# Kernel optimization log

Measured on AMD Instinct MI355X. Metric: run time of the kernel, lower is better.

## Reference

```python
import jax, jax.numpy as jnp
import numpy as np

N = 262144   # total nodes
E = 1048576  # total edges
B = 512      # graphs per batch
IN, H, EDIM, AH, CH, NB = 8, 128, 4, 128, 128, 4

def _lin(key, fi, fo):
    # kaiming_normal fan_out/relu approximated with fan_in scaling (only affects init stats)
    return jax.random.normal(key, (fi, fo), jnp.float32) * np.sqrt(2.0 / fi)

def setup_inputs() -> dict:
    key = jax.random.key(0)
    ks = jax.random.split(key, 24)
    inp = {}
    inp['x'] = jax.random.normal(ks[0], (N, IN), jnp.float32)
    inp['edge_index'] = jax.random.randint(ks[1], (2, E), 0, N)
    inp['edge_attr'] = jax.random.normal(ks[2], (E, EDIM), jnp.float32)
    seg = N // B
    inp['batch'] = (jnp.arange(N) // seg).astype(jnp.int32)
    inp['ptr'] = (jnp.arange(B + 1) * seg).astype(jnp.int32)
    dims = [(IN, H), (H, H), (H, H)]  # final layer outputs embed_dim == H
    for l, (di, do) in enumerate(dims):
        inp[f'We{l}'] = _lin(ks[3 + 2 * l], EDIM, di)
        inp[f'be{l}'] = jnp.zeros((di,), jnp.float32)
        inp[f'W{l}'] = _lin(ks[4 + 2 * l], di, do)
        inp[f'b{l}'] = jnp.zeros((do,), jnp.float32)
    inp['laW1'] = _lin(ks[10], H, AH); inp['lab1'] = jnp.zeros((AH,), jnp.float32)
    inp['laW2'] = _lin(ks[11], AH, 1); inp['lab2'] = jnp.zeros((1,), jnp.float32)
    inp['maW1'] = _lin(ks[12], H, AH); inp['mab1'] = jnp.zeros((AH,), jnp.float32)
    inp['maW2'] = _lin(ks[13], AH, NB); inp['mab2'] = jnp.zeros((NB,), jnp.float32)
    inp['lcW1'] = _lin(ks[14], H, CH); inp['lcb1'] = jnp.zeros((CH,), jnp.float32)
    inp['lcW2'] = _lin(ks[15], CH, 1); inp['lcb2'] = jnp.zeros((1,), jnp.float32)
    inp['mcW1'] = _lin(ks[16], H, CH); inp['mcb1'] = jnp.zeros((CH,), jnp.float32)
    inp['mcW2'] = _lin(ks[17], CH, 1); inp['mcb2'] = jnp.zeros((1,), jnp.float32)
    return inp

def _gnn(x, edge_index, edge_attr, Wes, bes, Ws, bs):
    # GINE-style edge-conditioned message passing (dropout off / eval mode)
    src, dst = edge_index[0], edge_index[1]
    h = x
    for We, be, W, b in zip(Wes, bes, Ws, bs):
        msg = jax.nn.relu(h[src] + edge_attr @ We + be)            # [E, d]
        agg = jax.ops.segment_sum(msg, dst, num_segments=N)        # [N, d]
        h = jax.nn.relu((h + agg) @ W + b)
    return h

def reference(x, edge_index, edge_attr, batch, ptr,
              We0, be0, W0, b0, We1, be1, W1, b1, We2, be2, W2, b2,
              laW1, lab1, laW2, lab2, maW1, mab1, maW2, mab2,
              lcW1, lcb1, lcW2, lcb2, mcW1, mcb1, mcW2, mcb2):
    emb = _gnn(x, edge_index, edge_attr, [We0, We1, We2], [be0, be1, be2], [W0, W1, W2], [b0, b1, b2])  # [N, H]

    # per-node location logit, then fused segmented softmax over each graph's nodes
    loc_logits = (jax.nn.relu(emb @ laW1 + lab1) @ laW2 + lab2)[:, 0]  # [N]
    seg_max = jax.ops.segment_max(loc_logits, batch, num_segments=B)
    shifted = loc_logits - seg_max[batch]
    denom = jax.ops.segment_sum(jnp.exp(shifted), batch, num_segments=B)
    logp = shifted - jnp.log(denom)[batch]                              # per-node log-prob within its graph
    loc_entropy = -jax.ops.segment_sum(jnp.exp(logp) * logp, batch, num_segments=B)  # [B]

    # segmented categorical sampling via Gumbel-max (global node index, matching start+local_idx)
    key = jax.random.key(42)
    u = jax.random.uniform(key, (N,), minval=1e-6, maxval=1.0 - 1e-6)
    pert = loc_logits - jnp.log(-jnp.log(u))
    pmax = jax.ops.segment_max(pert, batch, num_segments=B)
    cand = jnp.where(pert >= pmax[batch], jnp.arange(N), N)
    locations = jax.ops.segment_min(cand, batch, num_segments=B)        # [B] global indices
    loc_log_probs = logp[locations]                                     # [B]

    sel = emb[locations]                                                # [B, H]
    mut_logits = jax.nn.relu(sel @ maW1 + mab1) @ maW2 + mab2           # [B, NB]
    mut_logp = jax.nn.log_softmax(mut_logits, axis=-1)
    mutations = jax.random.categorical(jax.random.fold_in(key, 1), mut_logits, axis=-1)  # [B]
    mut_log_probs = jnp.take_along_axis(mut_logp, mutations[:, None], axis=-1)[:, 0]
    mut_entropy = -jnp.sum(jnp.exp(mut_logp) * mut_logp, axis=-1)

    # critics: global_add_pool + MLP -> scalar per graph; mutation critic on selected node
    pooled = jax.ops.segment_sum(emb, batch, num_segments=B)            # [B, H]
    loc_values = (jax.nn.relu(pooled @ lcW1 + lcb1) @ lcW2 + lcb2)[:, 0]
    mut_values = (jax.nn.relu(sel @ mcW1 + mcb1) @ mcW2 + mcb2)[:, 0]

    return (locations, mutations, loc_log_probs, mut_log_probs,
            loc_entropy, mut_entropy, loc_values, mut_values, emb)
```

## Files before the change

kernel.cpp:

```cpp
#include <hip/hip_runtime.h>
#include <cstdint>
#include <cstddef>

#define NN 262144
#define EE 1048576
#define BB 512
#define SEG 512

__device__ __forceinline__ unsigned rotl32(unsigned x, int r) {
    return (x << r) | (x >> (32 - r));
}

__device__ __forceinline__ void tf2x32(unsigned k0, unsigned k1, unsigned x0, unsigned x1,
                                       unsigned& o0, unsigned& o1) {
    unsigned ks[3] = {k0, k1, k0 ^ k1 ^ 0x1BD11BDAu};
    x0 += ks[0]; x1 += ks[1];
    const int R0[4] = {13, 15, 26, 6};
    const int R1[4] = {17, 29, 16, 24};
#pragma unroll
    for (int i = 0; i < 5; ++i) {
        const int* R = (i & 1) ? R1 : R0;
#pragma unroll
        for (int j = 0; j < 4; ++j) {
            x0 += x1;
            x1 = rotl32(x1, R[j]);
            x1 ^= x0;
        }
        x0 += ks[(i + 1) % 3];
        x1 += ks[(i + 2) % 3] + (unsigned)(i + 1);
    }
    o0 = x0; o1 = x1;
}

__device__ __forceinline__ float unif_loc(unsigned idx) {
    unsigned j = idx & (NN / 2 - 1);
    unsigned half = idx >> 17;
    unsigned o0, o1;
    tf2x32(0u, 42u, j, j + (unsigned)(NN / 2), o0, o1);
    unsigned bits = half ? o1 : o0;
    float f = __uint_as_float((bits >> 9) | 0x3F800000u) - 1.0f;
    const float minv = 1e-6f;
    const float maxv = 1.0f - 1e-6f;
    const float span = maxv - minv;
    return fmaxf(minv, __fadd_rn(__fmul_rn(f, span), minv));
}

__global__ void csr_count(const int* __restrict__ dst, int* __restrict__ counts, int E) {
    int i = blockIdx.x * 256 + threadIdx.x;
    if (i < E) atomicAdd(&counts[dst[i]], 1);
}

__global__ void scan512(const int* __restrict__ in, int* __restrict__ outExcl, int* __restrict__ bsum) {
    __shared__ int s[512];
    int b = blockIdx.x, tid = threadIdx.x;
    int v = in[(size_t)b * 512 + tid];
    s[tid] = v;
    __syncthreads();
    for (int d = 1; d < 512; d <<= 1) {
        int add = (tid >= d) ? s[tid - d] : 0;
        __syncthreads();
        s[tid] += add;
        __syncthreads();
    }
    outExcl[(size_t)b * 512 + tid] = s[tid] - v;
    if (tid == 511) bsum[b] = s[511];
}

__global__ void scan_fix(int* __restrict__ offs, const int* __restrict__ bbase,
                         int* __restrict__ cursor, int N, int E) {
    int gid = blockIdx.x * 512 + threadIdx.x;
    int v = offs[gid] + bbase[blockIdx.x];
    offs[gid] = v;
    cursor[gid] = v;
    if (gid == 0) offs[N] = E;
}

__global__ void csr_fill(const int* __restrict__ dst, const int* __restrict__ src,
                         const float4* __restrict__ ea, int* __restrict__ cursor,
                         int* __restrict__ ssrc, float4* __restrict__ sea, int E) {
    int i = blockIdx.x * 256 + threadIdx.x;
    if (i < E) {
        int p = atomicAdd(&cursor[dst[i]], 1);
        ssrc[p] = src[i];
        sea[p] = ea[i];
    }
}

__global__ void agg_l0(const float* __restrict__ x, const int* __restrict__ ssrc,
                       const float4* __restrict__ sea, const int* __restrict__ offs,
                       const float* __restrict__ We0, const float* __restrict__ be0,
                       float* __restrict__ out) {
    __shared__ float Ws[32];
    __shared__ float bs[8];
    int tid = threadIdx.x;
    if (tid < 32) Ws[tid] = We0[tid];
    if (tid < 8) bs[tid] = be0[tid];
    __syncthreads();
    int n = blockIdx.x * 256 + tid;
    float a[8] = {0.f, 0.f, 0.f, 0.f, 0.f, 0.f, 0.f, 0.f};
    int pb = offs[n], pe = offs[n + 1];
    for (int p = pb; p < pe; ++p) {
        int s = ssrc[p];
        float4 ev = sea[p];
        float4 xa = *(const float4*)(x + (size_t)s * 8);
        float4 xb = *(const float4*)(x + (size_t)s * 8 + 4);
        float xs[8] = {xa.x, xa.y, xa.z, xa.w, xb.x, xb.y, xb.z, xb.w};
#pragma unroll
        for (int j2 = 0; j2 < 8; ++j2) {
            float m = xs[j2] + bs[j2] + ev.x * Ws[j2] + ev.y * Ws[8 + j2] +
                      ev.z * Ws[16 + j2] + ev.w * Ws[24 + j2];
            a[j2] += fmaxf(m, 0.f);
        }
    }
    float4 o0 = {a[0], a[1], a[2], a[3]};
    float4 o1 = {a[4], a[5], a[6], a[7]};
    *(float4*)(out + (size_t)n * 8) = o0;
    *(float4*)(out + (size_t)n * 8 + 4) = o1;
}

__global__ void update_l0(const float* __restrict__ x, const float* __restrict__ agg0,
                          const float* __restrict__ W0, const float* __restrict__ b0,
                          float* __restrict__ h1) {
    __shared__ float Ws[8 * 128];
    __shared__ float bs[128];
    __shared__ float ts[2][8];
    int tid = threadIdx.x;
#pragma unroll
    for (int i = tid; i < 1024; i += 256) Ws[i] = W0[i];
    if (tid < 128) bs[tid] = b0[tid];
    int sub = tid >> 7;
    int c = tid & 127;
    int node = blockIdx.x * 2 + sub;
    if (c < 8) ts[sub][c] = x[(size_t)node * 8 + c] + agg0[(size_t)node * 8 + c];
    __syncthreads();
    float acc = bs[c];
#pragma unroll
    for (int k = 0; k < 8; ++k) acc = fmaf(ts[sub][k], Ws[k * 128 + c], acc);
    h1[(size_t)node * 128 + c] = fmaxf(acc, 0.f);
}

#define MSG(hv, ev)                                                                 \
    {                                                                               \
        float mx = hv.x + bv.x + ev.x * w0.x + ev.y * w1.x + ev.z * w2.x + ev.w * w3.x; \
        float my = hv.y + bv.y + ev.x * w0.y + ev.y * w1.y + ev.z * w2.y + ev.w * w3.y; \
        acc.x += fmaxf(mx, 0.f);                                                    \
        acc.y += fmaxf(my, 0.f);                                                    \
    }

__global__ __launch_bounds__(256) void agg_l(const float2* __restrict__ h2,
                                             const int* __restrict__ ssrc,
                                             const float4* __restrict__ sea,
                                             const int* __restrict__ offs,
                                             const float* __restrict__ We,
                                             const float* __restrict__ be,
                                             float2* __restrict__ out) {
    int tid = threadIdx.x;
    int node = blockIdx.x * 4 + (tid >> 6);
    node = __builtin_amdgcn_readfirstlane(node);
    int lane = tid & 63;
    const float2* We2 = (const float2*)We;
    float2 w0 = We2[lane], w1 = We2[64 + lane], w2 = We2[128 + lane], w3 = We2[192 + lane];
    float2 bv = ((const float2*)be)[lane];
    float2 acc; acc.x = 0.f; acc.y = 0.f;
    int pb = offs[node], pe = offs[node + 1];
    int p = pb;
    for (; p + 4 <= pe; p += 4) {
        int s0 = ssrc[p], s1 = ssrc[p + 1], s2 = ssrc[p + 2], s3 = ssrc[p + 3];
        float4 e0 = sea[p], e1 = sea[p + 1], e2 = sea[p + 2], e3 = sea[p + 3];
        float2 ha = h2[(size_t)s0 * 64 + lane];
        float2 hb = h2[(size_t)s1 * 64 + lane];
        float2 hc = h2[(size_t)s2 * 64 + lane];
        float2 hd = h2[(size_t)s3 * 64 + lane];
        MSG(ha, e0) MSG(hb, e1) MSG(hc, e2) MSG(hd, e3)
    }
    for (; p < pe; ++p) {
        int s0 = ssrc[p];
        float4 e0 = sea[p];
        float2 ha = h2[(size_t)s0 * 64 + lane];
        MSG(ha, e0)
    }
    out[(size_t)node * 64 + lane] = acc;
}

__device__ __forceinline__ int wslot(int c) {
    return (c & 1) ? (16 + (((c >> 1) + 4) & 15)) : (c >> 1);
}

__global__ __launch_bounds__(256, 4) void gemm_k(const float* __restrict__ P, const float* Q,
                                                 const float* __restrict__ W,
                                                 const float* __restrict__ bias,
                                                 float* out) {
    __shared__ float As[32][132];
    __shared__ float Ws[32][128];
    int tid = threadIdx.x;
    int r0 = blockIdx.x * 128;
    int ty = tid >> 4, tx = tid & 15;
    int wo1 = 4 * tx;
    int wo2 = 64 + 4 * ((tx + 4) & 15);
    float acc[8][8] = {};
    for (int kc = 0; kc < 4; ++kc) {
        int k0 = kc * 32;
        __syncthreads();
#pragma unroll
        for (int i = 0; i < 4; ++i) {
            int f = tid + 256 * i;
            int r = f >> 3;
            int c4 = f & 7;
            size_t g = (size_t)(r0 + r) * 128 + k0 + 4 * c4;
            float4 pv = *(const float4*)(P + g);
            if (Q) {
                float4 qv = *(const float4*)(Q + g);
                pv.x += qv.x; pv.y += qv.y; pv.z += qv.z; pv.w += qv.w;
            }
            As[4 * c4 + 0][r] = pv.x;
            As[4 * c4 + 1][r] = pv.y;
            As[4 * c4 + 2][r] = pv.z;
            As[4 * c4 + 3][r] = pv.w;
        }
#pragma unroll
        for (int i = 0; i < 4; ++i) {
            int f = tid + 256 * i;
            int k = f >> 5;
            int c4 = f & 31;
            float4 wv = *(const float4*)(W + (size_t)(k0 + k) * 128 + 4 * c4);
            *(float4*)&Ws[k][4 * wslot(c4)] = wv;
        }
        __syncthreads();
#pragma unroll 4
        for (int k = 0; k < 32; ++k) {
            float4 a0 = *(const float4*)&As[k][8 * ty];
            float4 a1 = *(const float4*)&As[k][8 * ty + 4];
            float4 wv0 = *(const float4*)&Ws[k][wo1];
            float4 wv1 = *(const float4*)&Ws[k][wo2];
            float av[8] = {a0.x, a0.y, a0.z, a0.w, a1.x, a1.y, a1.z, a1.w};
            float wv[8] = {wv0.x, wv0.y, wv0.z, wv0.w, wv1.x, wv1.y, wv1.z, wv1.w};
#pragma unroll
            for (int m = 0; m < 8; ++m)
#pragma unroll
                for (int n = 0; n < 8; ++n)
                    acc[m][n] = fmaf(av[m], wv[n], acc[m][n]);
        }
    }
    float4 b0 = *(const float4*)(bias + 8 * tx);
    float4 b1 = *(const float4*)(bias + 8 * tx + 4);
#pragma unroll
    for (int m = 0; m < 8; ++m) {
        float4 o0, o1;
        o0.x = fmaxf(acc[m][0] + b0.x, 0.f);
        o0.y = fmaxf(acc[m][1] + b0.y, 0.f);
        o0.z = fmaxf(acc[m][2] + b0.z, 0.f);
        o0.w = fmaxf(acc[m][3] + b0.w, 0.f);
        o1.x = fmaxf(acc[m][4] + b1.x, 0.f);
        o1.y = fmaxf(acc[m][5] + b1.y, 0.f);
        o1.z = fmaxf(acc[m][6] + b1.z, 0.f);
        o1.w = fmaxf(acc[m][7] + b1.w, 0.f);
        size_t g = (size_t)(r0 + 8 * ty + m) * 128 + 8 * tx;
        *(float4*)(out + g) = o0;
        *(float4*)(out + g + 4) = o1;
    }
}

__global__ __launch_bounds__(256, 4) void gemm_logit(const float* __restrict__ P,
                                                     const float* __restrict__ W,
                                                     const float* __restrict__ bias,
                                                     const float* __restrict__ w2,
                                                     const float* __restrict__ b2,
                                                     float* __restrict__ L) {
    __shared__ float As[32][132];
    __shared__ float Ws[32][128];
    int tid = threadIdx.x;
    int r0 = blockIdx.x * 128;
    int ty = tid >> 4, tx = tid & 15;
    int wo1 = 4 * tx;
    int wo2 = 64 + 4 * ((tx + 4) & 15);
    float acc[8][8] = {};
    for (int kc = 0; kc < 4; ++kc) {
        int k0 = kc * 32;
        __syncthreads();
#pragma unroll
        for (int i = 0; i < 4; ++i) {
            int f = tid + 256 * i;
            int r = f >> 3;
            int c4 = f & 7;
            size_t g = (size_t)(r0 + r) * 128 + k0 + 4 * c4;
            float4 pv = *(const float4*)(P + g);
            As[4 * c4 + 0][r] = pv.x;
            As[4 * c4 + 1][r] = pv.y;
            As[4 * c4 + 2][r] = pv.z;
            As[4 * c4 + 3][r] = pv.w;
        }
#pragma unroll
        for (int i = 0; i < 4; ++i) {
            int f = tid + 256 * i;
            int k = f >> 5;
            int c4 = f & 31;
            float4 wv = *(const float4*)(W + (size_t)(k0 + k) * 128 + 4 * c4);
            *(float4*)&Ws[k][4 * wslot(c4)] = wv;
        }
        __syncthreads();
#pragma unroll 4
        for (int k = 0; k < 32; ++k) {
            float4 a0 = *(const float4*)&As[k][8 * ty];
            float4 a1 = *(const float4*)&As[k][8 * ty + 4];
            float4 wv0 = *(const float4*)&Ws[k][wo1];
            float4 wv1 = *(const float4*)&Ws[k][wo2];
            float av[8] = {a0.x, a0.y, a0.z, a0.w, a1.x, a1.y, a1.z, a1.w};
            float wv[8] = {wv0.x, wv0.y, wv0.z, wv0.w, wv1.x, wv1.y, wv1.z, wv1.w};
#pragma unroll
            for (int m = 0; m < 8; ++m)
#pragma unroll
                for (int n = 0; n < 8; ++n)
                    acc[m][n] = fmaf(av[m], wv[n], acc[m][n]);
        }
    }
    float4 b0 = *(const float4*)(bias + 8 * tx);
    float4 b1 = *(const float4*)(bias + 8 * tx + 4);
    float4 w2a = *(const float4*)(w2 + 8 * tx);
    float4 w2b = *(const float4*)(w2 + 8 * tx + 4);
    float b2v = b2[0];
#pragma unroll
    for (int m = 0; m < 8; ++m) {
        float v = fmaxf(acc[m][0] + b0.x, 0.f) * w2a.x;
        v += fmaxf(acc[m][1] + b0.y, 0.f) * w2a.y;
        v += fmaxf(acc[m][2] + b0.z, 0.f) * w2a.z;
        v += fmaxf(acc[m][3] + b0.w, 0.f) * w2a.w;
        v += fmaxf(acc[m][4] + b1.x, 0.f) * w2b.x;
        v += fmaxf(acc[m][5] + b1.y, 0.f) * w2b.y;
        v += fmaxf(acc[m][6] + b1.z, 0.f) * w2b.z;
        v += fmaxf(acc[m][7] + b1.w, 0.f) * w2b.w;
        v += __shfl_down(v, 8, 16);
        v += __shfl_down(v, 4, 16);
        v += __shfl_down(v, 2, 16);
        v += __shfl_down(v, 1, 16);
        if (tx == 0) L[r0 + 8 * ty + m] = v + b2v;
    }
}

__global__ void sample_k(const float* __restrict__ L, float* __restrict__ ob,
                         int* __restrict__ locInt) {
    int g = blockIdx.x, tid = threadIdx.x;
    __shared__ float sh[512];
    __shared__ float rb[256];
    __shared__ int ib[256];
    float l0 = L[g * 512 + tid];
    float l1 = L[g * 512 + 256 + tid];
    rb[tid] = fmaxf(l0, l1);
    __syncthreads();
    for (int s2 = 128; s2 > 0; s2 >>= 1) {
        if (tid < s2) rb[tid] = fmaxf(rb[tid], rb[tid + s2]);
        __syncthreads();
    }
    float mx = rb[0];
    __syncthreads();
    float s0 = l0 - mx, s1 = l1 - mx;
    sh[tid] = s0; sh[256 + tid] = s1;
    float e0 = expf(s0), e1 = expf(s1);
    rb[tid] = e0 + e1;
    __syncthreads();
    for (int s2 = 128; s2 > 0; s2 >>= 1) {
        if (tid < s2) rb[tid] += rb[tid + s2];
        __syncthreads();
    }
    float denom = rb[0];
    __syncthreads();
    rb[tid] = e0 * s0 + e1 * s1;
    __syncthreads();
    for (int s2 = 128; s2 > 0; s2 >>= 1) {
        if (tid < s2) rb[tid] += rb[tid + s2];
        __syncthreads();
    }
    float sum2 = rb[0];
    __syncthreads();
    unsigned i0 = (unsigned)(g * 512 + tid);
    unsigned i1 = i0 + 256u;
    float p0 = l0 - logf(-logf(unif_loc(i0)));
    float p1 = l1 - logf(-logf(unif_loc(i1)));
    rb[tid] = fmaxf(p0, p1);
    __syncthreads();
    for (int s2 = 128; s2 > 0; s2 >>= 1) {
        if (tid < s2) rb[tid] = fmaxf(rb[tid], rb[tid + s2]);
        __syncthreads();
    }
    float pmax = rb[0];
    __syncthreads();
    int c0 = (p0 >= pmax) ? tid : 0x7FFFFFFF;
    int c1 = (p1 >= pmax) ? (tid + 256) : 0x7FFFFFFF;
    ib[tid] = min(c0, c1);
    __syncthreads();
    for (int s2 = 128; s2 > 0; s2 >>= 1) {
        if (tid < s2) ib[tid] = min(ib[tid], ib[tid + s2]);
        __syncthreads();
    }
    if (tid == 0) {
        int li = ib[0];
        float logD = logf(denom);
        ob[g] = (float)(g * 512 + li);
        ob[1024 + g] = sh[li] - logD;
        ob[2048 + g] = logD - sum2 / denom;
        locInt[g] = g * 512 + li;
    }
}

__global__ void pool_k(const float* __restrict__ emb, float* __restrict__ pooled) {
    int g = blockIdx.x, tid = threadIdx.x;
    int c = tid & 127, rg = tid >> 7;
    __shared__ float sh[512];
    float s0 = 0.f, s1 = 0.f, s2 = 0.f, s3 = 0.f;
    const float* base = emb + ((size_t)g * 512 + (size_t)rg * 128) * 128 + c;
    for (int n = 0; n < 128; n += 4) {
        s0 += base[(size_t)(n + 0) * 128];
        s1 += base[(size_t)(n + 1) * 128];
        s2 += base[(size_t)(n + 2) * 128];
        s3 += base[(size_t)(n + 3) * 128];
    }
    sh[tid] = (s0 + s1) + (s2 + s3);
    __syncthreads();
    if (rg == 0) pooled[g * 128 + c] = sh[c] + sh[128 + c] + sh[256 + c] + sh[384 + c];
}

__global__ void heads_k(const float* __restrict__ emb, const float* __restrict__ pooled,
                        const int* __restrict__ locInt,
                        const float* __restrict__ maW1, const float* __restrict__ mab1,
                        const float* __restrict__ maW2, const float* __restrict__ mab2,
                        const float* __restrict__ lcW1, const float* __restrict__ lcb1,
                        const float* __restrict__ lcW2, const float* __restrict__ lcb2,
                        const float* __restrict__ mcW1, const float* __restrict__ mcb1,
                        const float* __restrict__ mcW2, const float* __restrict__ mcb2,
                        float* __restrict__ ob) {
    int g = blockIdx.x, tid = threadIdx.x;
    __shared__ float sel[128], pl[128];
    __shared__ float red[4][128];
    __shared__ float red1[128];
    __shared__ float mcv_sh;
    sel[tid] = emb[(size_t)locInt[g] * 128 + tid];
    pl[tid] = pooled[g * 128 + tid];
    __syncthreads();
    float h = mab1[tid];
    for (int k = 0; k < 128; ++k) h = fmaf(sel[k], maW1[k * 128 + tid], h);
    h = fmaxf(h, 0.f);
    red[0][tid] = h * maW2[tid * 4 + 0];
    red[1][tid] = h * maW2[tid * 4 + 1];
    red[2][tid] = h * maW2[tid * 4 + 2];
    red[3][tid] = h * maW2[tid * 4 + 3];
    __syncthreads();
    for (int s2 = 64; s2 > 0; s2 >>= 1) {
        if (tid < s2) {
            red[0][tid] += red[0][tid + s2];
            red[1][tid] += red[1][tid + s2];
            red[2][tid] += red[2][tid + s2];
            red[3][tid] += red[3][tid + s2];
        }
        __syncthreads();
    }
    float h2 = mcb1[tid];
    for (int k = 0; k < 128; ++k) h2 = fmaf(sel[k], mcW1[k * 128 + tid], h2);
    h2 = fmaxf(h2, 0.f);
    red1[tid] = h2 * mcW2[tid];
    __syncthreads();
    for (int s2 = 64; s2 > 0; s2 >>= 1) {
        if (tid < s2) red1[tid] += red1[tid + s2];
        __syncthreads();
    }
    if (tid == 0) mcv_sh = red1[0] + mcb2[0];
    __syncthreads();
    float h3 = lcb1[tid];
    for (int k = 0; k < 128; ++k) h3 = fmaf(pl[k], lcW1[k * 128 + tid], h3);
    h3 = fmaxf(h3, 0.f);
    red1[tid] = h3 * lcW2[tid];
    __syncthreads();
    for (int s2 = 64; s2 > 0; s2 >>= 1) {
        if (tid < s2) red1[tid] += red1[tid + s2];
        __syncthreads();
    }
    if (tid == 0) {
        float lcv = red1[0] + lcb2[0];
        float lg[4];
#pragma unroll
        for (int c = 0; c < 4; ++c) lg[c] = red[c][0] + mab2[c];
        unsigned fk0, fk1;
        tf2x32(0u, 42u, 0u, 1u, fk0, fk1);
        float gmb[4];
#pragma unroll
        for (int c = 0; c < 4; ++c) {
            unsigned m = (unsigned)(g * 4 + c);
            unsigned j = m & 1023u;
            unsigned halfb = m >> 10;
            unsigned o0, o1;
            tf2x32(fk0, fk1, j, j + 1024u, o0, o1);
            unsigned bits = halfb ? o1 : o0;
            float f = __uint_as_float((bits >> 9) | 0x3F800000u) - 1.0f;
            const float tiny = 1.17549435e-38f;
            float u = fmaxf(tiny, __fadd_rn(__fmul_rn(f, 1.0f), tiny));
            gmb[c] = -logf(-logf(u));
        }
        int best = 0;
        float bz = gmb[0] + lg[0];
#pragma unroll
        for (int c = 1; c < 4; ++c) {
            float z = gmb[c] + lg[c];
            if (z > bz) { bz = z; best = c; }
        }
        float M = fmaxf(fmaxf(lg[0], lg[1]), fmaxf(lg[2], lg[3]));
        float se = 0.f;
#pragma unroll
        for (int c = 0; c < 4; ++c) se += expf(lg[c] - M);
        float lse = M + logf(se);
        float ent = 0.f;
#pragma unroll
        for (int c = 0; c < 4; ++c) {
            float lp = lg[c] - lse;
            ent -= expf(lp) * lp;
        }
        ob[512 + g] = (float)best;
        ob[1536 + g] = lg[best] - lse;
        ob[2560 + g] = ent;
        ob[3072 + g] = lcv;
        ob[3584 + g] = mcv_sh;
    }
}

extern "C" void kernel_launch(void* const* d_in, const int* in_sizes, int n_in,
                              void* d_out, int out_size, void* d_ws, size_t ws_size,
                              hipStream_t stream) {
    const float* x   = (const float*)d_in[0];
    const int* ei    = (const int*)d_in[1];
    const float* ea  = (const float*)d_in[2];
    const float* We0 = (const float*)d_in[5];
    const float* be0 = (const float*)d_in[6];
    const float* W0  = (const float*)d_in[7];
    const float* b0  = (const float*)d_in[8];
    const float* We1 = (const float*)d_in[9];
    const float* be1 = (const float*)d_in[10];
    const float* W1  = (const float*)d_in[11];
    const float* b1  = (const float*)d_in[12];
    const float* We2 = (const float*)d_in[13];
    const float* be2 = (const float*)d_in[14];
    const float* W2  = (const float*)d_in[15];
    const float* b2  = (const float*)d_in[16];
    const float* laW1 = (const float*)d_in[17];
    const float* lab1 = (const float*)d_in[18];
    const float* laW2 = (const float*)d_in[19];
    const float* lab2 = (const float*)d_in[20];
    const float* maW1 = (const float*)d_in[21];
    const float* mab1 = (const float*)d_in[22];
    const float* maW2 = (const float*)d_in[23];
    const float* mab2 = (const float*)d_in[24];
    const float* lcW1 = (const float*)d_in[25];
    const float* lcb1 = (const float*)d_in[26];
    const float* lcW2 = (const float*)d_in[27];
    const float* lcb2 = (const float*)d_in[28];
    const float* mcW1 = (const float*)d_in[29];
    const float* mcb1 = (const float*)d_in[30];
    const float* mcW2 = (const float*)d_in[31];
    const float* mcb2 = (const float*)d_in[32];

    float* out = (float*)d_out;
    char* ws = (char*)d_ws;
    size_t off = 0;
    auto alloc = [&](size_t bytes) -> void* {
        void* p = ws + off;
        off += (bytes + 255) & ~(size_t)255;
        return p;
    };
    float* U    = (float*)alloc((size_t)NN * 128 * 4);
    int* counts = (int*)alloc((size_t)NN * 4);
    int* offs   = (int*)alloc((size_t)(NN + 1) * 4);
    int* cursor = (int*)alloc((size_t)NN * 4);
    int* ssrc   = (int*)alloc((size_t)EE * 4);
    float4* sea = (float4*)alloc((size_t)EE * 16);
    int* bsum   = (int*)alloc(512 * 4);
    int* bbase  = (int*)alloc(512 * 4);
    int* bscr   = (int*)alloc(512 * 4);
    float* Lg   = (float*)alloc((size_t)NN * 4);
    float* pooled = (float*)alloc((size_t)BB * 128 * 4);
    int* locInt = (int*)alloc((size_t)BB * 4);

    const int* src = ei;
    const int* dstA = ei + EE;
    float* V = out + 4096;
    float* agg0 = U;

    hipMemsetAsync(counts, 0, (size_t)NN * 4, stream);
    csr_count<<<EE / 256, 256, 0, stream>>>(dstA, counts, EE);
    scan512<<<NN / 512, 512, 0, stream>>>(counts, offs, bsum);
    scan512<<<1, 512, 0, stream>>>(bsum, bbase, bscr);
    scan_fix<<<NN / 512, 512, 0, stream>>>(offs, bbase, cursor, NN, EE);
    csr_fill<<<EE / 256, 256, 0, stream>>>(dstA, src, (const float4*)ea, cursor, ssrc, sea, EE);

    agg_l0<<<NN / 256, 256, 0, stream>>>(x, ssrc, sea, offs, We0, be0, agg0);
    update_l0<<<NN / 2, 256, 0, stream>>>(x, agg0, W0, b0, V);
    agg_l<<<NN / 4, 256, 0, stream>>>((const float2*)V, ssrc, sea, offs, We1, be1, (float2*)U);
    gemm_k<<<NN / 128, 256, 0, stream>>>(V, U, W1, b1, U);
    agg_l<<<NN / 4, 256, 0, stream>>>((const float2*)U, ssrc, sea, offs, We2, be2, (float2*)V);
    gemm_k<<<NN / 128, 256, 0, stream>>>(U, V, W2, b2, V);

    gemm_logit<<<NN / 128, 256, 0, stream>>>(V, laW1, lab1, laW2, lab2, Lg);
    sample_k<<<BB, 256, 0, stream>>>(Lg, out, locInt);

    pool_k<<<BB, 512, 0, stream>>>(V, pooled);
    heads_k<<<BB, 128, 0, stream>>>(V, pooled, locInt, maW1, mab1, maW2, mab2,
                                    lcW1, lcb1, lcW2, lcb2, mcW1, mcb1, mcW2, mcb2, out);
}
```

Before: 1.017 ms.

## Fuse final GEMM with logit head, half-wave aggregation, async LDS weight loads

Fuses the last GNN update GEMM with the location-logit MLP so each block reuses its freshly written embedding tile instead of launching a separate pass. The aggregation kernel now processes two nodes per wavefront with float4 feature loads, looping to the larger degree of the pair with masking. The shared GEMM body loads weights directly into LDS via global_load_lds and prefetches the next A chunk into registers to overlap loads with compute. The divergent-degree masking wastes some work, and the fused kernel raises register and LDS pressure.

```diff
diff --git a/kernel.cpp b/kernel.cpp
--- a/kernel.cpp
+++ b/kernel.cpp
@@ -45,6 +45,11 @@
     return fmaxf(minv, __fadd_rn(__fmul_rn(f, span), minv));
 }
 
+__device__ __forceinline__ void gload_lds16(const float* g, float* l) {
+    __builtin_amdgcn_global_load_lds((const __attribute__((address_space(1))) unsigned int*)g,
+                                     (__attribute__((address_space(3))) unsigned int*)l, 16, 0, 0);
+}
+
 __global__ void csr_count(const int* __restrict__ dst, int* __restrict__ counts, int E) {
     int i = blockIdx.x * 256 + threadIdx.x;
     if (i < E) atomicAdd(&counts[dst[i]], 1);
@@ -139,77 +144,78 @@
     h1[(size_t)node * 128 + c] = fmaxf(acc, 0.f);
 }
 
-#define MSG(hv, ev)                                                                 \
-    {                                                                               \
-        float mx = hv.x + bv.x + ev.x * w0.x + ev.y * w1.x + ev.z * w2.x + ev.w * w3.x; \
-        float my = hv.y + bv.y + ev.x * w0.y + ev.y * w1.y + ev.z * w2.y + ev.w * w3.y; \
-        acc.x += fmaxf(mx, 0.f);                                                    \
-        acc.y += fmaxf(my, 0.f);                                                    \
-    }
-
-__global__ __launch_bounds__(256) void agg_l(const float2* __restrict__ h2,
+__global__ __launch_bounds__(256) void agg_l(const float* __restrict__ h,
                                              const int* __restrict__ ssrc,
                                              const float4* __restrict__ sea,
                                              const int* __restrict__ offs,
                                              const float* __restrict__ We,
                                              const float* __restrict__ be,
-                                             float2* __restrict__ out) {
+                                             float* __restrict__ out) {
     int tid = threadIdx.x;
-    int node = blockIdx.x * 4 + (tid >> 6);
-    node = __builtin_amdgcn_readfirstlane(node);
     int lane = tid & 63;
-    const float2* We2 = (const float2*)We;
-    float2 w0 = We2[lane], w1 = We2[64 + lane], w2 = We2[128 + lane], w3 = We2[192 + lane];
-    float2 bv = ((const float2*)be)[lane];
-    float2 acc; acc.x = 0.f; acc.y = 0.f;
+    int half = lane >> 5;
+    int dl = lane & 31;
+    int node = blockIdx.x * 8 + (tid >> 6) * 2 + half;
+    float4 w0 = *(const float4*)(We + 4 * dl);
+    float4 w1 = *(const float4*)(We + 128 + 4 * dl);
+    float4 w2 = *(const float4*)(We + 256 + 4 * dl);
+    float4 w3 = *(const float4*)(We + 384 + 4 * dl);
+    float4 bv = *(const float4*)(be + 4 * dl);
     int pb = offs[node], pe = offs[node + 1];
-    int p = pb;
-    for (; p + 4 <= pe; p += 4) {
-        int s0 = ssrc[p], s1 = ssrc[p + 1], s2 = ssrc[p + 2], s3 = ssrc[p + 3];
-        float4 e0 = sea[p], e1 = sea[p + 1], e2 = sea[p + 2], e3 = sea[p + 3];
-        float2 ha = h2[(size_t)s0 * 64 + lane];
-        float2 hb = h2[(size_t)s1 * 64 + lane];
-        float2 hc = h2[(size_t)s2 * 64 + lane];
-        float2 hd = h2[(size_t)s3 * 64 + lane];
-        MSG(ha, e0) MSG(hb, e1) MSG(hc, e2) MSG(hd, e3)
-    }
-    for (; p < pe; ++p) {
-        int s0 = ssrc[p];
-        float4 e0 = sea[p];
-        float2 ha = h2[(size_t)s0 * 64 + lane];
-        MSG(ha, e0)
-    }
-    out[(size_t)node * 64 + lane] = acc;
-}
-
-__device__ __forceinline__ int wslot(int c) {
-    return (c & 1) ? (16 + (((c >> 1) + 4) & 15)) : (c >> 1);
-}
-
-__global__ __launch_bounds__(256, 4) void gemm_k(const float* __restrict__ P, const float* Q,
-                                                 const float* __restrict__ W,
-                                                 const float* __restrict__ bias,
-                                                 float* out) {
-    __shared__ float As[32][132];
-    __shared__ float Ws[32][128];
-    int tid = threadIdx.x;
-    int r0 = blockIdx.x * 128;
-    int ty = tid >> 4, tx = tid & 15;
-    int wo1 = 4 * tx;
-    int wo2 = 64 + 4 * ((tx + 4) & 15);
-    float acc[8][8] = {};
+    int deg = pe - pb;
+    int dmax = max(deg, __shfl_xor(deg, 32, 64));
+    float4 acc = {0.f, 0.f, 0.f, 0.f};
+    for (int t = 0; t < dmax; ++t) {
+        int p = pb + t;
+        bool act = p < pe;
+        int pc = min(p, max(pe - 1, 0));
+        int s = ssrc[pc];
+        float4 ev = sea[pc];
+        float4 hv = *(const float4*)(h + (size_t)s * 128 + 4 * dl);
+        float4 m;
+        m.x = hv.x + bv.x + ev.x * w0.x + ev.y * w1.x + ev.z * w2.x + ev.w * w3.x;
+        m.y = hv.y + bv.y + ev.x * w0.y + ev.y * w1.y + ev.z * w2.y + ev.w * w3.y;
+        m.z = hv.z + bv.z + ev.x * w0.z + ev.y * w1.z + ev.z * w2.z + ev.w * w3.z;
+        m.w = hv.w + bv.w + ev.x * w0.w + ev.y * w1.w + ev.z * w2.w + ev.w * w3.w;
+        acc.x += act ? fmaxf(m.x, 0.f) : 0.f;
+        acc.y += act ? fmaxf(m.y, 0.f) : 0.f;
+        acc.z += act ? fmaxf(m.z, 0.f) : 0.f;
+        acc.w += act ? fmaxf(m.w, 0.f) : 0.f;
+    }
+    *(float4*)(out + (size_t)node * 128 + 4 * dl) = acc;
+}
+
+__device__ __forceinline__ void mm_pass(const float* __restrict__ P, const float* Q,
+                                        const float* __restrict__ W,
+                                        float (&As)[32][132], float (&Ws)[32][128],
+                                        float (&acc)[8][8], int r0) {
+    const int tid = threadIdx.x;
+    const int ty = tid >> 4, tx = tid & 15;
+    const int lane = tid & 63, wv = tid >> 6;
+    float4 pa[4], qa[4];
+#pragma unroll
+    for (int i = 0; i < 4; ++i) {
+        int f = tid + 256 * i;
+        int r = f >> 3, c4 = f & 7;
+        size_t g = (size_t)(r0 + r) * 128 + 4 * c4;
+        pa[i] = *(const float4*)(P + g);
+        if (Q) qa[i] = *(const float4*)(Q + g);
+    }
     for (int kc = 0; kc < 4; ++kc) {
-        int k0 = kc * 32;
-        __syncthreads();
+        const int k0 = kc * 32;
+        __syncthreads();
+#pragma unroll
+        for (int i = 0; i < 4; ++i) {
+            int kRow = 8 * wv + 2 * i;
+            gload_lds16(W + (size_t)(k0 + kRow) * 128 + 4 * lane, &Ws[kRow][0]);
+        }
 #pragma unroll
         for (int i = 0; i < 4; ++i) {
             int f = tid + 256 * i;
-            int r = f >> 3;
-            int c4 = f & 7;
-            size_t g = (size_t)(r0 + r) * 128 + k0 + 4 * c4;
-            float4 pv = *(const float4*)(P + g);
+            int r = f >> 3, c4 = f & 7;
+            float4 pv = pa[i];
             if (Q) {
-                float4 qv = *(const float4*)(Q + g);
+                float4 qv = qa[i];
                 pv.x += qv.x; pv.y += qv.y; pv.z += qv.z; pv.w += qv.w;
             }
             As[4 * c4 + 0][r] = pv.x;
@@ -217,32 +223,46 @@
             As[4 * c4 + 2][r] = pv.z;
             As[4 * c4 + 3][r] = pv.w;
         }
-#pragma unroll
-        for (int i = 0; i < 4; ++i) {
-            int f = tid + 256 * i;
-            int k = f >> 5;
-            int c4 = f & 31;
-            float4 wv = *(const float4*)(W + (size_t)(k0 + k) * 128 + 4 * c4);
-            *(float4*)&Ws[k][4 * wslot(c4)] = wv;
-        }
-        __syncthreads();
+        __syncthreads();
+        if (kc < 3) {
+#pragma unroll
+            for (int i = 0; i < 4; ++i) {
+                int f = tid + 256 * i;
+                int r = f >> 3, c4 = f & 7;
+                size_t g = (size_t)(r0 + r) * 128 + (k0 + 32) + 4 * c4;
+                pa[i] = *(const float4*)(P + g);
+                if (Q) qa[i] = *(const float4*)(Q + g);
+            }
+        }
 #pragma unroll 4
         for (int k = 0; k < 32; ++k) {
             float4 a0 = *(const float4*)&As[k][8 * ty];
             float4 a1 = *(const float4*)&As[k][8 * ty + 4];
-            float4 wv0 = *(const float4*)&Ws[k][wo1];
-            float4 wv1 = *(const float4*)&Ws[k][wo2];
+            float4 w0 = *(const float4*)&Ws[k][4 * tx];
+            float4 w1 = *(const float4*)&Ws[k][64 + 4 * tx];
             float av[8] = {a0.x, a0.y, a0.z, a0.w, a1.x, a1.y, a1.z, a1.w};
-            float wv[8] = {wv0.x, wv0.y, wv0.z, wv0.w, wv1.x, wv1.y, wv1.z, wv1.w};
+            float wn[8] = {w0.x, w0.y, w0.z, w0.w, w1.x, w1.y, w1.z, w1.w};
 #pragma unroll
             for (int m = 0; m < 8; ++m)
 #pragma unroll
                 for (int n = 0; n < 8; ++n)
-                    acc[m][n] = fmaf(av[m], wv[n], acc[m][n]);
-        }
-    }
-    float4 b0 = *(const float4*)(bias + 8 * tx);
-    float4 b1 = *(const float4*)(bias + 8 * tx + 4);
+                    acc[m][n] = fmaf(av[m], wn[n], acc[m][n]);
+        }
+    }
+}
+
+__global__ __launch_bounds__(256, 4) void gemm_k(const float* __restrict__ P, const float* Q,
+                                                 const float* __restrict__ W,
+                                                 const float* __restrict__ bias,
+                                                 float* __restrict__ out) {
+    __shared__ float As[32][132];
+    __shared__ float Ws[32][128];
+    int r0 = blockIdx.x * 128;
+    int ty = threadIdx.x >> 4, tx = threadIdx.x & 15;
+    float acc[8][8] = {};
+    mm_pass(P, Q, W, As, Ws, acc, r0);
+    float4 b0 = *(const float4*)(bias + 4 * tx);
+    float4 b1 = *(const float4*)(bias + 64 + 4 * tx);
 #pragma unroll
     for (int m = 0; m < 8; ++m) {
         float4 o0, o1;
@@ -254,85 +274,69 @@
         o1.y = fmaxf(acc[m][5] + b1.y, 0.f);
         o1.z = fmaxf(acc[m][6] + b1.z, 0.f);
         o1.w = fmaxf(acc[m][7] + b1.w, 0.f);
-        size_t g = (size_t)(r0 + 8 * ty + m) * 128 + 8 * tx;
-        *(float4*)(out + g) = o0;
-        *(float4*)(out + g + 4) = o1;
-    }
-}
-
-__global__ __launch_bounds__(256, 4) void gemm_logit(const float* __restrict__ P,
-                                                     const float* __restrict__ W,
-                                                     const float* __restrict__ bias,
-                                                     const float* __restrict__ w2,
-                                                     const float* __restrict__ b2,
-                                                     float* __restrict__ L) {
+        size_t g = (size_t)(r0 + 8 * ty + m) * 128;
+        *(float4*)(out + g + 4 * tx) = o0;
+        *(float4*)(out + g + 64 + 4 * tx) = o1;
+    }
+}
+
+__global__ __launch_bounds__(256, 4) void gemm_emb_logit(
+        const float* __restrict__ P, const float* Q,
+        const float* __restrict__ W, const float* __restrict__ bias,
+        float* __restrict__ emb,
+        const float* __restrict__ aW1, const float* __restrict__ ab1,
+        const float* __restrict__ aW2, const float* __restrict__ ab2,
+        float* __restrict__ L) {
     __shared__ float As[32][132];
     __shared__ float Ws[32][128];
-    int tid = threadIdx.x;
     int r0 = blockIdx.x * 128;
-    int ty = tid >> 4, tx = tid & 15;
-    int wo1 = 4 * tx;
-    int wo2 = 64 + 4 * ((tx + 4) & 15);
-    float acc[8][8] = {};
-    for (int kc = 0; kc < 4; ++kc) {
-        int k0 = kc * 32;
-        __syncthreads();
-#pragma unroll
-        for (int i = 0; i < 4; ++i) {
-            int f = tid + 256 * i;
-            int r = f >> 3;
-            int c4 = f & 7;
-            size_t g = (size_t)(r0 + r) * 128 + k0 + 4 * c4;
-            float4 pv = *(const float4*)(P + g);
-            As[4 * c4 + 0][r] = pv.x;
-            As[4 * c4 + 1][r] = pv.y;
-            As[4 * c4 + 2][r] = pv.z;
-            As[4 * c4 + 3][r] = pv.w;
-        }
-#pragma unroll
-        for (int i = 0; i < 4; ++i) {
-            int f = tid + 256 * i;
-            int k = f >> 5;
-            int c4 = f & 31;
-            float4 wv = *(const float4*)(W + (size_t)(k0 + k) * 128 + 4 * c4);
-            *(float4*)&Ws[k][4 * wslot(c4)] = wv;
-        }
-        __syncthreads();
-#pragma unroll 4
-        for (int k = 0; k < 32; ++k) {
-            float4 a0 = *(const float4*)&As[k][8 * ty];
-            float4 a1 = *(const float4*)&As[k][8 * ty + 4];
-            float4 wv0 = *(const float4*)&Ws[k][wo1];
-            float4 wv1 = *(const float4*)&Ws[k][wo2];
-            float av[8] = {a0.x, a0.y, a0.z, a0.w, a1.x, a1.y, a1.z, a1.w};
-            float wv[8] = {wv0.x, wv0.y, wv0.z, wv0.w, wv1.x, wv1.y, wv1.z, wv1.w};
-#pragma unroll
-            for (int m = 0; m < 8; ++m)
-#pragma unroll
-                for (int n = 0; n < 8; ++n)
-                    acc[m][n] = fmaf(av[m], wv[n], acc[m][n]);
-        }
-    }
-    float4 b0 = *(const float4*)(bias + 8 * tx);
-    float4 b1 = *(const float4*)(bias + 8 * tx + 4);
-    float4 w2a = *(const float4*)(w2 + 8 * tx);
-    float4 w2b = *(const float4*)(w2 + 8 * tx + 4);
-    float b2v = b2[0];
-#pragma unroll
-    for (int m = 0; m < 8; ++m) {
-        float v = fmaxf(acc[m][0] + b0.x, 0.f) * w2a.x;
-        v += fmaxf(acc[m][1] + b0.y, 0.f) * w2a.y;
-        v += fmaxf(acc[m][2] + b0.z, 0.f) * w2a.z;
-        v += fmaxf(acc[m][3] + b0.w, 0.f) * w2a.w;
-        v += fmaxf(acc[m][4] + b1.x, 0.f) * w2b.x;
-        v += fmaxf(acc[m][5] + b1.y, 0.f) * w2b.y;
-        v += fmaxf(acc[m][6] + b1.z, 0.f) * w2b.z;
-        v += fmaxf(acc[m][7] + b1.w, 0.f) * w2b.w;
-        v += __shfl_down(v, 8, 16);
-        v += __shfl_down(v, 4, 16);
-        v += __shfl_down(v, 2, 16);
-        v += __shfl_down(v, 1, 16);
-        if (tx == 0) L[r0 + 8 * ty + m] = v + b2v;
+    int ty = threadIdx.x >> 4, tx = threadIdx.x & 15;
+    {
+        float acc[8][8] = {};
+        mm_pass(P, Q, W, As, Ws, acc, r0);
+        float4 b0 = *(const float4*)(bias + 4 * tx);
+        float4 b1 = *(const float4*)(bias + 64 + 4 * tx);
+#pragma unroll
+        for (int m = 0; m < 8; ++m) {
+            float4 o0, o1;
+            o0.x = fmaxf(acc[m][0] + b0.x, 0.f);
+            o0.y = fmaxf(acc[m][1] + b0.y, 0.f);
+            o0.z = fmaxf(acc[m][2] + b0.z, 0.f);
+            o0.w = fmaxf(acc[m][3] + b0.w, 0.f);
+            o1.x = fmaxf(acc[m][4] + b1.x, 0.f);
+            o1.y = fmaxf(acc[m][5] + b1.y, 0.f);
+            o1.z = fmaxf(acc[m][6] + b1.z, 0.f);
+            o1.w = fmaxf(acc[m][7] + b1.w, 0.f);
+            size_t g = (size_t)(r0 + 8 * ty + m) * 128;
+            *(float4*)(emb + g + 4 * tx) = o0;
+            *(float4*)(emb + g + 64 + 4 * tx) = o1;
+        }
+    }
+    __syncthreads();
+    {
+        float acc[8][8] = {};
+        mm_pass(emb, nullptr, aW1, As, Ws, acc, r0);
+        float4 b0 = *(const float4*)(ab1 + 4 * tx);
+        float4 b1 = *(const float4*)(ab1 + 64 + 4 * tx);
+        float4 wa = *(const float4*)(aW2 + 4 * tx);
+        float4 wb = *(const float4*)(aW2 + 64 + 4 * tx);
+        float b2v = ab2[0];
+#pragma unroll
+        for (int m = 0; m < 8; ++m) {
+            float v = fmaxf(acc[m][0] + b0.x, 0.f) * wa.x;
+            v += fmaxf(acc[m][1] + b0.y, 0.f) * wa.y;
+            v += fmaxf(acc[m][2] + b0.z, 0.f) * wa.z;
+            v += fmaxf(acc[m][3] + b0.w, 0.f) * wa.w;
+            v += fmaxf(acc[m][4] + b1.x, 0.f) * wb.x;
+            v += fmaxf(acc[m][5] + b1.y, 0.f) * wb.y;
+            v += fmaxf(acc[m][6] + b1.z, 0.f) * wb.z;
+            v += fmaxf(acc[m][7] + b1.w, 0.f) * wb.w;
+            v += __shfl_down(v, 8, 16);
+            v += __shfl_down(v, 4, 16);
+            v += __shfl_down(v, 2, 16);
+            v += __shfl_down(v, 1, 16);
+            if (tx == 0) L[r0 + 8 * ty + m] = v + b2v;
+        }
     }
 }
 
@@ -589,14 +593,12 @@
 
     agg_l0<<<NN / 256, 256, 0, stream>>>(x, ssrc, sea, offs, We0, be0, agg0);
     update_l0<<<NN / 2, 256, 0, stream>>>(x, agg0, W0, b0, V);
-    agg_l<<<NN / 4, 256, 0, stream>>>((const float2*)V, ssrc, sea, offs, We1, be1, (float2*)U);
+    agg_l<<<NN / 8, 256, 0, stream>>>(V, ssrc, sea, offs, We1, be1, U);
     gemm_k<<<NN / 128, 256, 0, stream>>>(V, U, W1, b1, U);
-    agg_l<<<NN / 4, 256, 0, stream>>>((const float2*)U, ssrc, sea, offs, We2, be2, (float2*)V);
-    gemm_k<<<NN / 128, 256, 0, stream>>>(U, V, W2, b2, V);
-
-    gemm_logit<<<NN / 128, 256, 0, stream>>>(V, laW1, lab1, laW2, lab2, Lg);
+    agg_l<<<NN / 8, 256, 0, stream>>>(U, ssrc, sea, offs, We2, be2, V);
+    gemm_emb_logit<<<NN / 128, 256, 0, stream>>>(U, V, W2, b2, V,
+                                                 laW1, lab1, laW2, lab2, Lg);
     sample_k<<<BB, 256, 0, stream>>>(Lg, out, locInt);
-
     pool_k<<<BB, 512, 0, stream>>>(V, pooled);
     heads_k<<<BB, 128, 0, stream>>>(V, pooled, locInt, maW1, mab1, maW2, mab2,
                                     lcW1, lcb1, lcW2, lcb2, mcW1, mcb1, mcW2, mcb2, out);
```

New measurement: 1.190 ms. +17.1%, slower.
